# Kernel tuning notes

Hardware: AMD Instinct MI355X
Metric: run time of the kernel (lower is better)

Reference implementation:

```python
import jax, jax.numpy as jnp
import numpy as np

TEMP = 0.07
N, D = 4096, 1024


def setup_inputs() -> dict:
    key = jax.random.key(0)
    k1, k2 = jax.random.split(key)
    z1 = jax.random.normal(k1, (N, D), dtype=jnp.float32)
    z2 = jax.random.normal(k2, (N, D), dtype=jnp.float32)
    # docstring says embeddings are normalized
    z1 = z1 / jnp.linalg.norm(z1, axis=1, keepdims=True)
    z2 = z2 / jnp.linalg.norm(z2, axis=1, keepdims=True)
    return {"z1": z1, "z2": z2}


def reference(z1, z2):
    n = z1.shape[0]
    z = jnp.concatenate([z1, z2], axis=0)          # [2N, D]
    sim = jnp.matmul(z, z.T) / TEMP                # [2N, 2N]
    # mask self-similarity (diagonal) with -inf, as in masked_fill_
    self_mask = jnp.eye(2 * n, dtype=bool)
    sim = jnp.where(self_mask, -jnp.inf, sim)
    # positive sims: sim[i, i+N] for i<N and sim[i, i-N] for i>=N,
    # i.e. the diagonal of z1@z2.T repeated for both halves
    pos = jnp.sum(z1 * z2, axis=1) / TEMP          # [N]
    pos = jnp.concatenate([pos, pos], axis=0)      # [2N]
    # denominator: logsumexp over sim with ONLY self masked (positives included),
    # matching the original torch code (neg_sim is computed but unused)
    lse = jax.nn.logsumexp(sim, axis=1)            # [2N]
    return jnp.mean(-pos + lse)
```

## Files before the change

### kernel.cpp

```cpp
#include <hip/hip_runtime.h>
#include <hip/hip_bf16.h>


typedef __attribute__((ext_vector_type(4))) int i32x4;
typedef __attribute__((ext_vector_type(8))) int i32x8;
typedef __attribute__((ext_vector_type(16))) float f32x16;

#define NN 4096
#define TWO_N 8192
#define DIM 1024
#define TEMP_INV 14.285714285714286f
#define EXP_SCALE 20.609929155566303f
#define NT 64
#define NBLK 2080
#define SLOTB 16384

#define GLD16(g, l)                                                          \
  __builtin_amdgcn_global_load_lds(                                          \
      (const __attribute__((address_space(1))) void*)(g),                    \
      (__attribute__((address_space(3))) void*)(l), 16, 0, 0)

__global__ __launch_bounds__(256) void prep_kernel(
    const float* __restrict__ z1, const float* __restrict__ z2,
    unsigned int* __restrict__ zf8, float* __restrict__ pos) {
  const int row = blockIdx.x, t = threadIdx.x;
  float4 a = ((const float4*)(z1 + (size_t)row * DIM))[t];
  float4 b = ((const float4*)(z2 + (size_t)row * DIM))[t];
  int wa = __builtin_amdgcn_cvt_pk_fp8_f32(a.x, a.y, 0, false);
  wa = __builtin_amdgcn_cvt_pk_fp8_f32(a.z, a.w, wa, true);
  int wb = __builtin_amdgcn_cvt_pk_fp8_f32(b.x, b.y, 0, false);
  wb = __builtin_amdgcn_cvt_pk_fp8_f32(b.z, b.w, wb, true);
  zf8[(size_t)row * (DIM / 4) + t] = (unsigned int)wa;
  zf8[(size_t)(NN + row) * (DIM / 4) + t] = (unsigned int)wb;
  float s = a.x * b.x + a.y * b.y + a.z * b.z + a.w * b.w;
#pragma unroll
  for (int off = 1; off < 64; off <<= 1) s += __shfl_xor(s, off);
  __shared__ float tmp[4];
  if ((t & 63) == 0) tmp[t >> 6] = s;
  __syncthreads();
  if (t == 0) pos[row] = (tmp[0] + tmp[1] + tmp[2] + tmp[3]) * TEMP_INV;
}

__global__ __launch_bounds__(256, 4) void lse_kernel(
    const unsigned char* __restrict__ zb8, float* __restrict__ part) {
  __shared__ unsigned char lds[2 * SLOTB];
  int u = ((int)blockIdx.x & 7) * (NBLK / 8) + ((int)blockIdx.x >> 3);
  int I = 0, rem = u;
  while (rem >= NT - I) { rem -= NT - I; ++I; }
  const int J = I + rem;
  const int rowA0 = I * 128, colB0 = J * 128;
  const bool diag = (I == J);

  const int t = threadIdx.x;
  const int wave = t >> 6, lane = t & 63;
  const int wm = wave >> 1, wn = wave & 1;
  const int l31 = lane & 31, kh = lane >> 5;

  int oA[2], oB[2];
#pragma unroll
  for (int i = 0; i < 2; ++i) {
    int c = i * 256 + t, row = c >> 2, p = c & 3;
    oA[i] = (rowA0 + row) * DIM + (p ^ ((row >> 1) & 3)) * 16;
    oB[i] = (colB0 + row) * DIM + (p ^ ((row >> 1) & 3)) * 16;
  }

  const int arow_l = wm * 64 + l31;
  const int brow_l = wn * 64 + l31;

  f32x16 acc[2][2];
#pragma unroll
  for (int m = 0; m < 2; ++m)
#pragma unroll
    for (int n = 0; n < 2; ++n)
#pragma unroll
      for (int r = 0; r < 16; ++r) acc[m][n][r] = 0.f;

#define STAGE(dst_, k_)                                                       \
  {                                                                           \
    const unsigned char* gk = zb8 + ((k_) & 15) * 64;                         \
    GLD16(gk + oA[0], (dst_) + wave * 1024);                                  \
    GLD16(gk + oA[1], (dst_) + 4096 + wave * 1024);                           \
    GLD16(gk + oB[0], (dst_) + 8192 + wave * 1024);                           \
    GLD16(gk + oB[1], (dst_) + 8192 + 4096 + wave * 1024);                    \
  }

#define READ_FRAG(F, base_, rloc_)                                            \
  {                                                                           \
    const unsigned char* rb_ = (base_) + (rloc_) * 64;                        \
    const int cls_ = ((rloc_) >> 1) & 3;                                      \
    i32x4 lo_ = *(const i32x4*)(rb_ + (((2 * kh) ^ cls_) << 4));              \
    i32x4 hi_ = *(const i32x4*)(rb_ + (((2 * kh + 1) ^ cls_) << 4));          \
    F[0] = lo_[0]; F[1] = lo_[1]; F[2] = lo_[2]; F[3] = lo_[3];               \
    F[4] = hi_[0]; F[5] = hi_[1]; F[6] = hi_[2]; F[7] = hi_[3];               \
  }

  unsigned char* cur = lds;
  unsigned char* oth = lds + SLOTB;

  STAGE(cur, 0);
  asm volatile("s_waitcnt vmcnt(0)" ::: "memory");

#pragma unroll 1
  for (int s = 0; s < DIM / 64; ++s) {
    __builtin_amdgcn_s_barrier();
    __builtin_amdgcn_sched_barrier(0);
    STAGE(oth, s + 1);
    asm volatile("s_waitcnt vmcnt(4)" ::: "memory");
    __builtin_amdgcn_s_barrier();
    __builtin_amdgcn_sched_barrier(0);

    i32x8 a0, a1, b0, b1;
    READ_FRAG(a0, cur, arow_l);
    READ_FRAG(a1, cur, arow_l + 32);
    READ_FRAG(b0, cur + 8192, brow_l);
    READ_FRAG(b1, cur + 8192, brow_l + 32);
    __builtin_amdgcn_s_setprio(1);
    acc[0][0] = __builtin_amdgcn_mfma_scale_f32_32x32x64_f8f6f4(
        a0, b0, acc[0][0], 0, 0, 0, 127, 0, 127);
    acc[0][1] = __builtin_amdgcn_mfma_scale_f32_32x32x64_f8f6f4(
        a0, b1, acc[0][1], 0, 0, 0, 127, 0, 127);
    acc[1][0] = __builtin_amdgcn_mfma_scale_f32_32x32x64_f8f6f4(
        a1, b0, acc[1][0], 0, 0, 0, 127, 0, 127);
    acc[1][1] = __builtin_amdgcn_mfma_scale_f32_32x32x64_f8f6f4(
        a1, b1, acc[1][1], 0, 0, 0, 127, 0, 127);
    __builtin_amdgcn_s_setprio(0);
    unsigned char* tmp_ = cur; cur = oth; oth = tmp_;
  }
  asm volatile("s_waitcnt vmcnt(0) lgkmcnt(0)" ::: "memory");

  float* rplane = part + (size_t)(2 * J + wn) * TWO_N;
  float* cplane = part + (size_t)(128 + 2 * I + wm) * TWO_N;
  float csum[2] = {0.f, 0.f};
#pragma unroll
  for (int m = 0; m < 2; ++m) {
#pragma unroll
    for (int r = 0; r < 16; ++r) {
      const int grow = rowA0 + wm * 64 + m * 32 + (r & 3) + 8 * (r >> 2) + 4 * kh;
      float s = 0.f;
#pragma unroll
      for (int n = 0; n < 2; ++n) {
        const int gcol = colB0 + wn * 64 + n * 32 + l31;
        float e = exp2f((acc[m][n][r] - 1.0f) * EXP_SCALE);
        if (grow == gcol) e = 0.f;
        s += e;
        csum[n] += e;
      }
      s += __shfl_xor(s, 1); s += __shfl_xor(s, 2); s += __shfl_xor(s, 4);
      s += __shfl_xor(s, 8); s += __shfl_xor(s, 16);
      if (l31 == 0) rplane[grow] = s;
    }
  }
  if (!diag) {
#pragma unroll
    for (int n = 0; n < 2; ++n) {
      float c = csum[n];
      c += __shfl_xor(c, 32);
      if (lane < 32) cplane[colB0 + wn * 64 + n * 32 + lane] = c;
    }
  }
#undef READ_FRAG
#undef STAGE
}

__global__ __launch_bounds__(256) void reduce_finalize_kernel(
    const float* __restrict__ part, const float* __restrict__ pos,
    float* __restrict__ out) {
  const int i = blockIdx.x * 256 + threadIdx.x;
  const int Ji = i >> 7;
  float s = 0.f;
  for (int J = Ji; J < NT; ++J)
    s += part[(size_t)(2 * J) * TWO_N + i] + part[(size_t)(2 * J + 1) * TWO_N + i];
  for (int I = 0; I < Ji; ++I)
    s += part[(size_t)(128 + 2 * I) * TWO_N + i] +
         part[(size_t)(128 + 2 * I + 1) * TWO_N + i];
  float term = TEMP_INV + logf(s) - pos[i & (NN - 1)];
#pragma unroll
  for (int off = 1; off < 64; off <<= 1) term += __shfl_xor(term, off);
  __shared__ float tmp[4];
  const int t = threadIdx.x;
  if ((t & 63) == 0) tmp[t >> 6] = term;
  __syncthreads();
  if (t == 0)
    atomicAdd(out, (tmp[0] + tmp[1] + tmp[2] + tmp[3]) * (1.0f / (float)TWO_N));
}

extern "C" void kernel_launch(void* const* d_in, const int* in_sizes, int n_in,
                              void* d_out, int out_size, void* d_ws, size_t ws_size,
                              hipStream_t stream) {
  const float* z1 = (const float*)d_in[0];
  const float* z2 = (const float*)d_in[1];
  float* out = (float*)d_out;

  char* ws = (char*)d_ws;
  unsigned char* zf8 = (unsigned char*)ws;
  size_t off = (size_t)TWO_N * DIM;
  float* part = (float*)(ws + off);
  off += (size_t)256 * TWO_N * 4;
  float* pos = (float*)(ws + off);

  hipMemsetAsync(out, 0, sizeof(float), stream);
  prep_kernel<<<NN, 256, 0, stream>>>(z1, z2, (unsigned int*)zf8, pos);
  lse_kernel<<<NBLK, 256, 0, stream>>>(zf8, part);
  reduce_finalize_kernel<<<TWO_N / 256, 256, 0, stream>>>(part, pos, out);
}
```

Measured before the change: 96.27 us.

## Re-swizzle LDS tile layout per 32-row block and parallelize partial-sum reduction

Changes the global-to-LDS staging so each 32-row block is stored contiguously with an XOR swizzle keyed on the row index. Fragment reads now use a precomputed per-lane offset, which simplifies address math and is meant to reduce LDS bank conflicts. The reduce kernel now gives each column 8 thread groups that each cover 32 of the partial planes, with a shared-memory combine, and launches 256 blocks instead of 32. This raises parallelism in the final reduction at the cost of extra shared-memory traffic and more atomics on the output.

```diff
diff --git a/kernel.cpp b/kernel.cpp
--- a/kernel.cpp
+++ b/kernel.cpp
@@ -59,13 +59,15 @@
   int oA[2], oB[2];
 #pragma unroll
   for (int i = 0; i < 2; ++i) {
-    int c = i * 256 + t, row = c >> 2, p = c & 3;
-    oA[i] = (rowA0 + row) * DIM + (p ^ ((row >> 1) & 3)) * 16;
-    oB[i] = (colB0 + row) * DIM + (p ^ ((row >> 1) & 3)) * 16;
-  }
-
-  const int arow_l = wm * 64 + l31;
-  const int brow_l = wn * 64 + l31;
+    int c = i * 256 + t, rb = c >> 7, l = (c >> 2) & 31, w = c & 3;
+    int kk = w ^ (l & 3);
+    oA[i] = (rowA0 + rb * 32 + l) * DIM + kk * 16;
+    oB[i] = (colB0 + rb * 32 + l) * DIM + kk * 16;
+  }
+
+  const int lrow64 = l31 * 64;
+  const int cls = l31 & 3;
+  const int x2kh = 2 * kh;
 
   f32x16 acc[2][2];
 #pragma unroll
@@ -81,15 +83,14 @@
     GLD16(gk + oA[0], (dst_) + wave * 1024);                                  \
     GLD16(gk + oA[1], (dst_) + 4096 + wave * 1024);                           \
     GLD16(gk + oB[0], (dst_) + 8192 + wave * 1024);                           \
-    GLD16(gk + oB[1], (dst_) + 8192 + 4096 + wave * 1024);                    \
-  }
-
-#define READ_FRAG(F, base_, rloc_)                                            \
+    GLD16(gk + oB[1], (dst_) + 12288 + wave * 1024);                          \
+  }
+
+#define READ_FRAG(F, base_, rb_)                                              \
   {                                                                           \
-    const unsigned char* rb_ = (base_) + (rloc_) * 64;                        \
-    const int cls_ = ((rloc_) >> 1) & 3;                                      \
-    i32x4 lo_ = *(const i32x4*)(rb_ + (((2 * kh) ^ cls_) << 4));              \
-    i32x4 hi_ = *(const i32x4*)(rb_ + (((2 * kh + 1) ^ cls_) << 4));          \
+    const unsigned char* p_ = (base_) + (rb_) * 2048 + lrow64;                \
+    i32x4 lo_ = *(const i32x4*)(p_ + ((x2kh ^ cls) << 4));                    \
+    i32x4 hi_ = *(const i32x4*)(p_ + (((x2kh + 1) ^ cls) << 4));              \
     F[0] = lo_[0]; F[1] = lo_[1]; F[2] = lo_[2]; F[3] = lo_[3];               \
     F[4] = hi_[0]; F[5] = hi_[1]; F[6] = hi_[2]; F[7] = hi_[3];               \
   }
@@ -110,10 +111,10 @@
     __builtin_amdgcn_sched_barrier(0);
 
     i32x8 a0, a1, b0, b1;
-    READ_FRAG(a0, cur, arow_l);
-    READ_FRAG(a1, cur, arow_l + 32);
-    READ_FRAG(b0, cur + 8192, brow_l);
-    READ_FRAG(b1, cur + 8192, brow_l + 32);
+    READ_FRAG(a0, cur, wm * 2);
+    READ_FRAG(a1, cur, wm * 2 + 1);
+    READ_FRAG(b0, cur + 8192, wn * 2);
+    READ_FRAG(b1, cur + 8192, wn * 2 + 1);
     __builtin_amdgcn_s_setprio(1);
     acc[0][0] = __builtin_amdgcn_mfma_scale_f32_32x32x64_f8f6f4(
         a0, b0, acc[0][0], 0, 0, 0, 127, 0, 127);
@@ -165,23 +166,31 @@
 __global__ __launch_bounds__(256) void reduce_finalize_kernel(
     const float* __restrict__ part, const float* __restrict__ pos,
     float* __restrict__ out) {
-  const int i = blockIdx.x * 256 + threadIdx.x;
-  const int Ji = i >> 7;
-  float s = 0.f;
-  for (int J = Ji; J < NT; ++J)
-    s += part[(size_t)(2 * J) * TWO_N + i] + part[(size_t)(2 * J + 1) * TWO_N + i];
-  for (int I = 0; I < Ji; ++I)
-    s += part[(size_t)(128 + 2 * I) * TWO_N + i] +
-         part[(size_t)(128 + 2 * I + 1) * TWO_N + i];
-  float term = TEMP_INV + logf(s) - pos[i & (NN - 1)];
-#pragma unroll
-  for (int off = 1; off < 64; off <<= 1) term += __shfl_xor(term, off);
-  __shared__ float tmp[4];
   const int t = threadIdx.x;
-  if ((t & 63) == 0) tmp[t >> 6] = term;
+  const int tg = t >> 5, r = t & 31;
+  const int i = blockIdx.x * 32 + r;
+  const int Ji2 = 2 * (i >> 7);
+  const float* col = part + i;
+  float ssum = 0.f;
+#pragma unroll 8
+  for (int p = tg * 32; p < tg * 32 + 32; ++p) {
+    bool valid = (p < 128) ? (p >= Ji2) : ((p - 128) < Ji2);
+    if (valid) ssum += col[(size_t)p * TWO_N];
+  }
+  __shared__ float red[8][32];
+  red[tg][r] = ssum;
   __syncthreads();
-  if (t == 0)
-    atomicAdd(out, (tmp[0] + tmp[1] + tmp[2] + tmp[3]) * (1.0f / (float)TWO_N));
+  if (t < 32) {
+    float s = 0.f;
+#pragma unroll
+    for (int g = 0; g < 8; ++g) s += red[g][t];
+    const int i2 = blockIdx.x * 32 + t;
+    float term = TEMP_INV + logf(s) - pos[i2 & (NN - 1)];
+    term += __shfl_xor(term, 1); term += __shfl_xor(term, 2);
+    term += __shfl_xor(term, 4); term += __shfl_xor(term, 8);
+    term += __shfl_xor(term, 16);
+    if (t == 0) atomicAdd(out, term * (1.0f / (float)TWO_N));
+  }
 }
 
 extern "C" void kernel_launch(void* const* d_in, const int* in_sizes, int n_in,
@@ -201,5 +210,5 @@
   hipMemsetAsync(out, 0, sizeof(float), stream);
   prep_kernel<<<NN, 256, 0, stream>>>(z1, z2, (unsigned int*)zf8, pos);
   lse_kernel<<<NBLK, 256, 0, stream>>>(zf8, part);
-  reduce_finalize_kernel<<<TWO_N / 256, 256, 0, stream>>>(part, pos, out);
-}
+  reduce_finalize_kernel<<<TWO_N / 32, 256, 0, stream>>>(part, pos, out);
+}
```

New measurement: 99.21 us. 1.03x slower.
